# Optimization experiments

Measured on AMD Instinct MI355X. Metric: run time of the kernel, lower is better.

## Reference

```python
import jax, jax.numpy as jnp
import numpy as np

ALPHA = 0.3  # LeakyReLU negative slope
NEG_INF = -1e9


def setup_inputs() -> dict:
    key = jax.random.key(0)
    k1, k2, k3, k4 = jax.random.split(key, 4)
    B, N, C_IN, C_OUT, H = 4, 2048, 128, 128, 4
    node_feats = jax.random.normal(k1, (B, N, C_IN), dtype=jnp.float32)
    # xavier_uniform with gain 1.414 for projection weight [c_out, c_in]
    limit_w = 1.414 * np.sqrt(6.0 / (C_IN + C_OUT))
    W = jax.random.uniform(k2, (C_OUT, C_IN), minval=-limit_w, maxval=limit_w, dtype=jnp.float32)
    b = jnp.zeros((C_OUT,), dtype=jnp.float32)
    c_head = C_OUT // H
    limit_a = 1.414 * np.sqrt(6.0 / (H + 2 * c_head))
    a = jax.random.uniform(k3, (H, 2 * c_head), minval=-limit_a, maxval=limit_a, dtype=jnp.float32)
    return {"node_feats": node_feats, "W": W, "b": b, "a": a}


def reference(node_feats, W, b, a):
    B, N, _ = node_feats.shape
    H, two_c = a.shape
    c = two_c // 2
    # dynamic adjacency: cosine similarity, sigmoid > 0.5  <=>  sim > 0
    nf = node_feats / jnp.maximum(jnp.linalg.norm(node_feats, axis=-1, keepdims=True), 1e-12)
    sim = jnp.einsum('bid,bjd->bij', nf, nf)            # [B,N,N]
    mask = sim > 0.0                                     # adjacency (sigmoid(sim) > 0.5)
    # projection -> per-head features [B,N,H,c]
    h = (node_feats @ W.T + b).reshape(B, N, H, c)
    # edge score a . [h_i, h_j] decomposes into left/right parts
    a_l, a_r = a[:, :c], a[:, c:]                        # [H,c] each
    s_l = jnp.einsum('bnhc,hc->bnh', h, a_l)             # [B,N,H]
    s_r = jnp.einsum('bnhc,hc->bnh', h, a_r)             # [B,N,H]
    logits = jax.nn.leaky_relu(s_l[:, :, None, :] + s_r[:, None, :, :], ALPHA)  # [B,N,N,H]
    attn = jnp.where(mask[..., None], logits, NEG_INF)
    probs = jax.nn.softmax(attn, axis=2)                 # softmax over source nodes j
    # dropout is identity in eval mode
    out = jnp.einsum('bijh,bjhc->bihc', probs, h)
    return out.reshape(B, N, -1)                         # concat heads
```

## Files before the change

### kernel.cpp

```cpp
#include <hip/hip_runtime.h>
#include <cstdint>
#include <cstddef>

typedef float v16f __attribute__((ext_vector_type(16)));
typedef short v8s  __attribute__((ext_vector_type(8)));

#define MFMA32(A,B,C) __builtin_amdgcn_mfma_f32_32x32x16_bf16((A),(B),(C),0,0,0)
#define THRU 1e-3f

__device__ __forceinline__ unsigned f2bf(float f) {
  unsigned u = __builtin_bit_cast(unsigned, f);
  u += 0x7FFFu + ((u >> 16) & 1u);
  return u >> 16;
}
__device__ __forceinline__ float bf2f(unsigned us) {
  return __builtin_bit_cast(float, us << 16);
}
__device__ __forceinline__ void gload16(const void* g, void* l) {
  __builtin_amdgcn_global_load_lds(
      (const __attribute__((address_space(1))) void*)g,
      (__attribute__((address_space(3))) void*)l, 16, 0, 0);
}

__global__ __launch_bounds__(256) void gat_prep(
    const float* __restrict__ nf, const float* __restrict__ Wm,
    const float* __restrict__ bias, const float* __restrict__ aw,
    unsigned short* __restrict__ nfh, unsigned short* __restrict__ nfm,
    unsigned short* __restrict__ ht,
    float* __restrict__ EFl, float* __restrict__ EFrp)
{
  __shared__ float xl[32][132];
  const int tid = threadIdx.x;
  const int row = tid & 31, g = tid >> 5;
  const int r0 = blockIdx.x * 32;
  const int b = r0 >> 11, n0 = r0 & 2047;
  const int d0 = g * 16;

  float x[16];
  {
    const float* xp = nf + (size_t)(r0 + row) * 128 + d0;
#pragma unroll
    for (int q = 0; q < 4; ++q) {
      float4 v = *(const float4*)(xp + 4 * q);
      x[4*q+0] = v.x; x[4*q+1] = v.y; x[4*q+2] = v.z; x[4*q+3] = v.w;
    }
  }
  {
    unsigned hu[16], mu[16];
#pragma unroll
    for (int q = 0; q < 16; ++q) {
      xl[row][d0 + q] = x[q];
      unsigned hb = f2bf(x[q]); float hf = bf2f(hb);
      unsigned mb = f2bf(x[q] - hf);
      hu[q] = hb; mu[q] = mb;
    }
    const size_t to = ((size_t)(b * 64 + (n0 >> 5)) * 8 + g) * 512 + row * 8;
    uint4 p0, p1;
    p0.x = hu[0] | (hu[1] << 16);  p0.y = hu[2] | (hu[3] << 16);
    p0.z = hu[4] | (hu[5] << 16);  p0.w = hu[6] | (hu[7] << 16);
    p1.x = hu[8] | (hu[9] << 16);  p1.y = hu[10] | (hu[11] << 16);
    p1.z = hu[12] | (hu[13] << 16); p1.w = hu[14] | (hu[15] << 16);
    *(uint4*)(nfh + to) = p0; *(uint4*)(nfh + to + 256) = p1;
    p0.x = mu[0] | (mu[1] << 16);  p0.y = mu[2] | (mu[3] << 16);
    p0.z = mu[4] | (mu[5] << 16);  p0.w = mu[6] | (mu[7] << 16);
    p1.x = mu[8] | (mu[9] << 16);  p1.y = mu[10] | (mu[11] << 16);
    p1.z = mu[12] | (mu[13] << 16); p1.w = mu[14] | (mu[15] << 16);
    *(uint4*)(nfm + to) = p0; *(uint4*)(nfm + to + 256) = p1;
  }
  __syncthreads();

  float acc[16];
  const int ob = g * 16;
#pragma unroll
  for (int o = 0; o < 16; ++o) acc[o] = bias[ob + o];
  for (int dd = 0; dd < 128; dd += 4) {
    float4 xq = *(const float4*)&xl[row][dd];
#pragma unroll
    for (int o = 0; o < 16; ++o) {
      float4 wq = *(const float4*)(Wm + (size_t)(ob + o) * 128 + dd);
      acc[o] = fmaf(xq.x, wq.x, acc[o]);
      acc[o] = fmaf(xq.y, wq.y, acc[o]);
      acc[o] = fmaf(xq.z, wq.z, acc[o]);
      acc[o] = fmaf(xq.w, wq.w, acc[o]);
    }
  }
#pragma unroll
  for (int o = 0; o < 16; ++o)
    ht[((size_t)b * 128 + ob + o) * 2048 + n0 + row] = (unsigned short)f2bf(acc[o]);

  const int hh = g >> 1, cb = (g & 1) * 16;
  float sl = 0.f, sr = 0.f;
#pragma unroll
  for (int o = 0; o < 16; ++o) {
    sl = fmaf(acc[o], aw[hh * 64 + cb + o], sl);
    sr = fmaf(acc[o], aw[hh * 64 + 32 + cb + o], sr);
  }
  sl += __shfl_xor(sl, 32, 64);
  sr += __shfl_xor(sr, 32, 64);
  if (!(g & 1)) {
    const float L2E = 1.4426950408889634f;
    float El = exp2f(sl * L2E), Fl = exp2f(sl * (0.3f * L2E));
    float Er = exp2f(sr * L2E), Fr = exp2f(sr * (0.3f * L2E));
    size_t nn = (size_t)(r0 + row);
    EFl[nn * 8 + hh]     = El;
    EFl[nn * 8 + 4 + hh] = Fl;
    EFrp[nn * 8 + (hh >> 1) * 4 + (hh & 1) * 2]     = Er;
    EFrp[nn * 8 + (hh >> 1) * 4 + (hh & 1) * 2 + 1] = Fr;
  }
}

__global__ __launch_bounds__(256) void gat_mask(
    const unsigned short* __restrict__ nfh, const unsigned short* __restrict__ nfm,
    const float* __restrict__ nf, unsigned* __restrict__ mask)
{
  const int tid = threadIdx.x, lane = tid & 63;
  const int li = lane & 31, hi = lane >> 5;
  const int blk = blockIdx.x;
  const int jb = blk & 31, t = blk >> 5;
  const int ib = t & 15, b = t >> 4;
  const int i0 = ib * 128 + (tid >> 6) * 32;
  const int j0 = jb * 64;

  const size_t lbyte = (size_t)lane * 8;
  const size_t tiB  = ((size_t)(b * 64 + (i0 >> 5)) * 8) * 512 + lbyte;
  const size_t tjA0 = ((size_t)(b * 64 + (j0 >> 5)) * 8) * 512 + lbyte;
  const size_t tjA1 = tjA0 + 4096;

  v8s BH[8], BM[8];
#pragma unroll
  for (int kc = 0; kc < 8; ++kc) {
    BH[kc] = *(const v8s*)(nfh + tiB + kc * 512);
    BM[kc] = *(const v8s*)(nfm + tiB + kc * 512);
  }

  v16f S0, S1;
#pragma unroll
  for (int r = 0; r < 16; ++r) { S0[r] = 0.f; S1[r] = 0.f; }
#pragma unroll
  for (int kc = 0; kc < 8; ++kc) {
    v8s A0h = *(const v8s*)(nfh + tjA0 + kc * 512);
    v8s A1h = *(const v8s*)(nfh + tjA1 + kc * 512);
    v8s A0m = *(const v8s*)(nfm + tjA0 + kc * 512);
    v8s A1m = *(const v8s*)(nfm + tjA1 + kc * 512);
    S0 = MFMA32(A0h, BH[kc], S0);
    S1 = MFMA32(A1h, BH[kc], S1);
    S0 = MFMA32(A0h, BM[kc], S0);
    S1 = MFMA32(A1h, BM[kc], S1);
    S0 = MFMA32(A0m, BH[kc], S0);
    S1 = MFMA32(A1m, BH[kc], S1);
  }

  unsigned u0 = 0, u1 = 0;
  float mn = 1e30f;
  const int sh = hi * 4;
#pragma unroll
  for (int r = 0; r < 16; ++r) {
    const int jlc = (r & 3) + 8 * (r >> 2);
    const unsigned bit = (1u << jlc) << sh;
    if (S0[r] > 0.f) u0 |= bit;
    if (S1[r] > 0.f) u1 |= bit;
    mn = fminf(mn, fabsf(S0[r]));
    mn = fminf(mn, fabsf(S1[r]));
  }

  if (mn < THRU) {
    const float* xi = nf + ((size_t)b * 2048 + i0 + li) * 128;
#pragma unroll
    for (int sub = 0; sub < 2; ++sub) {
#pragma unroll
      for (int r = 0; r < 16; ++r) {
        const float s = sub ? S1[r] : S0[r];
        if (fabsf(s) < THRU) {
          const int jlc = (r & 3) + 8 * (r >> 2);
          const int j = j0 + sub * 32 + jlc + 4 * hi;
          const float* xj = nf + ((size_t)b * 2048 + j) * 128;
          double a = 0.0;
          for (int k = 0; k < 128; k += 2) {
            a = fma((double)xi[k],     (double)xj[k],     a);
            a = fma((double)xi[k + 1], (double)xj[k + 1], a);
          }
          const unsigned bit = (1u << jlc) << sh;
          if (sub == 0) u0 = (a > 0.0) ? (u0 | bit) : (u0 & ~bit);
          else          u1 = (a > 0.0) ? (u1 | bit) : (u1 & ~bit);
        }
      }
    }
  }

  unsigned f0 = u0 | (unsigned)__shfl_xor((int)u0, 32, 64);
  unsigned f1 = u1 | (unsigned)__shfl_xor((int)u1, 32, 64);
  if (hi == 0) {
    mask[(size_t)(b * 64 + jb * 2)     * 2048 + i0 + li] = f0;
    mask[(size_t)(b * 64 + jb * 2 + 1) * 2048 + i0 + li] = f1;
  }
}

#define PVBLK(pw, h, smv)                                                      \
  {                                                                            \
    auto q0 = __builtin_amdgcn_permlane32_swap((int)pw[0], (int)pw[2], false, false); \
    auto q1 = __builtin_amdgcn_permlane32_swap((int)pw[1], (int)pw[3], false, false); \
    auto q2 = __builtin_amdgcn_permlane32_swap((int)pw[4], (int)pw[6], false, false); \
    auto q3 = __builtin_amdgcn_permlane32_swap((int)pw[5], (int)pw[7], false, false); \
    uint4 c0, c1;                                                              \
    c0.x = (unsigned)q0[0]; c0.y = (unsigned)q1[0];                            \
    c0.z = (unsigned)q0[1]; c0.w = (unsigned)q1[1];                            \
    c1.x = (unsigned)q2[0]; c1.y = (unsigned)q3[0];                            \
    c1.z = (unsigned)q2[1]; c1.w = (unsigned)q3[1];                            \
    v8s P0 = __builtin_bit_cast(v8s, c0);                                      \
    v8s P1 = __builtin_bit_cast(v8s, c1);                                      \
    const int cc = (h) * 32 + li;                                              \
    const char* vr = (smv) + cc * 256;                                         \
    const int cx = cc & 15;                                                    \
    v8s V0 = *(const v8s*)(vr + ((((it2 << 2) + hi) ^ cx) << 4));              \
    v8s V1 = *(const v8s*)(vr + ((((it2 << 2) + 2 + hi) ^ cx) << 4));          \
    acc[h] = MFMA32(P0, V0, acc[h]);                                           \
    acc[h] = MFMA32(P1, V1, acc[h]);                                           \
  }

template<int CH>
__global__ __launch_bounds__(256, 2) void gat_attn(
    const unsigned short* __restrict__ ht, const float* __restrict__ EFl,
    const float* __restrict__ EFrp, const unsigned* __restrict__ mask,
    float* __restrict__ nump, float* __restrict__ denp)
{
  constexpr int JPC = 2048 / CH;
  constexpr int H = JPC >> 7;
  constexpr int MW = JPC >> 5;
  __shared__ __align__(16) char sm[2][18432];

  const int tid = threadIdx.x, lane = tid & 63, wv = tid >> 6;
  const int li = lane & 31, hi = lane >> 5;

  const int blk = blockIdx.x;
  const int x = blk & 7, y = blk >> 3;
  const int ig = y & 15;
  const int combo = x * CH + (y >> 4);
  const int hp2 = combo & 1;
  const int r2 = combo >> 1;
  const int ch = r2 % CH, b = r2 / CH;

  const size_t nb = (size_t)b * 2048;
  const int i0 = ig * 128 + wv * 32;
  const int j0 = ch * JPC;

  float EL[2], FL[2];
  {
    const float* p = EFl + (nb + i0 + li) * 8 + 2 * hp2;
    float2 e = *(const float2*)p;
    float2 f = *(const float2*)(p + 4);
    EL[0] = e.x; EL[1] = e.y; FL[0] = f.x; FL[1] = f.y;
  }

  unsigned mw[MW];
#pragma unroll
  for (int q = 0; q < MW; ++q)
    mw[q] = mask[(size_t)(b * 64 + (j0 >> 5) + q) * 2048 + i0 + li] >> (hi * 4);

  v16f acc[2];
#pragma unroll
  for (int h = 0; h < 2; ++h)
#pragma unroll
    for (int r = 0; r < 16; ++r) acc[h][r] = 0.f;
  float den[2] = {0.f, 0.f};

  auto STAGE = [&](int h0, int p) {
    const int jbase = j0 + (h0 << 7);
    const size_t cbase = (size_t)b * 128 + (hp2 << 6);
#pragma unroll
    for (int s = 0; s < 4; ++s) {
      const int L = s * 4096 + tid * 16;
      const int c = L >> 8, gs = (L >> 4) & 15;
      const int g = gs ^ (c & 15);
      gload16((const char*)ht + (((cbase + c) * 2048 + jbase) << 1) + (g << 4),
              sm[p] + L);
    }
    if (tid < 128)
      gload16((const char*)EFrp + (size_t)(nb + jbase + tid) * 32 + (hp2 << 4),
              sm[p] + 16384 + tid * 16);
  };

  STAGE(0, 0);
  __syncthreads();

#pragma unroll
  for (int h0 = 0; h0 < H; ++h0) {
    const int p = h0 & 1;
    if (h0) __syncthreads();
    if (h0 + 1 < H) STAGE(h0 + 1, p ^ 1);

#pragma unroll
    for (int it2 = 0; it2 < 4; ++it2) {
      const char* Eb = sm[p] + 16384 + (it2 << 9);
      const unsigned mh = mw[(h0 << 2) + it2];
      unsigned pA[8], pB[8];
#pragma unroll
      for (int rp = 0; rp < 8; ++rp) {
        const int r0 = 2 * rp;
        const int jl0c = (r0 & 3) + 8 * (r0 >> 2);
        const int nA = (jl0c + 4 * hi) * 16;
        float4 e0 = *(const float4*)(Eb + nA);
        float4 e1 = *(const float4*)(Eb + nA + 16);
        const bool m0 = (mh >> jl0c) & 1;
        const bool m1 = (mh >> (jl0c + 1)) & 1;
        float wA0 = fmaxf(e0.x * EL[0], e0.y * FL[0]); wA0 = m0 ? wA0 : 0.f;
        float wB0 = fmaxf(e0.z * EL[1], e0.w * FL[1]); wB0 = m0 ? wB0 : 0.f;
        float wA1 = fmaxf(e1.x * EL[0], e1.y * FL[0]); wA1 = m1 ? wA1 : 0.f;
        float wB1 = fmaxf(e1.z * EL[1], e1.w * FL[1]); wB1 = m1 ? wB1 : 0.f;
        den[0] += wA0 + wA1;
        den[1] += wB0 + wB1;
        asm("v_cvt_pk_bf16_f32 %0, %1, %2" : "=v"(pA[rp]) : "v"(wA0), "v"(wA1));
        asm("v_cvt_pk_bf16_f32 %0, %1, %2" : "=v"(pB[rp]) : "v"(wB0), "v"(wB1));
      }
      PVBLK(pA, 0, sm[p])
      PVBLK(pB, 1, sm[p])
    }
  }

#pragma unroll
  for (int h = 0; h < 2; ++h) den[h] += __shfl_xor(den[h], 32, 64);

  const size_t obase = ((size_t)b * CH + ch) * 2048 + i0;
#pragma unroll
  for (int h = 0; h < 2; ++h) {
#pragma unroll
    for (int r = 0; r < 16; ++r) {
      const int il = (r & 3) + 8 * (r >> 2) + 4 * hi;
      nump[(obase + il) * 128 + (hp2 * 2 + h) * 32 + li] = acc[h][r];
    }
  }
  if (lane < 32) {
    float2 dv; dv.x = den[0]; dv.y = den[1];
    *(float2*)(denp + (obase + li) * 4 + 2 * hp2) = dv;
  }
}

__global__ __launch_bounds__(256) void gat_reduce(
    const float* __restrict__ nump, const float* __restrict__ denp,
    float* __restrict__ out, const int CH)
{
  const int t = blockIdx.x * 256 + threadIdx.x;
  const int b = t >> 16;
  const int rem = t & 65535;
  const int n = rem >> 5;
  const int col = (rem & 31) * 4;
  const int h = col >> 5;
  float4 s = make_float4(0.f, 0.f, 0.f, 0.f);
  float d = 0.f;
  for (int ch = 0; ch < CH; ++ch) {
    const size_t rb = ((size_t)b * CH + ch) * 2048 + n;
    float4 v = *(const float4*)(nump + rb * 128 + col);
    s.x += v.x; s.y += v.y; s.z += v.z; s.w += v.w;
    d += denp[rb * 4 + h];
  }
  float4 o;
  o.x = s.x / d; o.y = s.y / d; o.z = s.z / d; o.w = s.w / d;
  *(float4*)(out + (size_t)t * 4) = o;
}

extern "C" void kernel_launch(void* const* d_in, const int* in_sizes, int n_in,
                              void* d_out, int out_size, void* d_ws, size_t ws_size,
                              hipStream_t stream) {
  const float* nf   = (const float*)d_in[0];
  const float* Wm   = (const float*)d_in[1];
  const float* bias = (const float*)d_in[2];
  const float* aw   = (const float*)d_in[3];
  float* out = (float*)d_out;
  char* ws = (char*)d_ws;

  unsigned short* nfh  = (unsigned short*)(ws);
  unsigned short* nfm  = (unsigned short*)(ws + 2097152);
  unsigned short* ht   = (unsigned short*)(ws + 4194304);
  float*    EFl  = (float*)(ws + 6291456);
  float*    EFrp = (float*)(ws + 6553600);
  unsigned* mask = (unsigned*)(ws + 6815744);
  const size_t o_den = 8912896;

  int CH = 8;
  if (ws_size < o_den + 8ull * 4325376ull) CH = 4;

  float* denp = (float*)(ws + o_den);
  float* nump = (float*)(ws + o_den + (size_t)CH * 131072);

  gat_prep<<<256, 256, 0, stream>>>(nf, Wm, bias, aw, nfh, nfm, ht, EFl, EFrp);
  gat_mask<<<2048, 256, 0, stream>>>(nfh, nfm, nf, mask);
  if (CH == 8)
    gat_attn<8><<<1024, 256, 0, stream>>>(ht, EFl, EFrp, mask, nump, denp);
  else
    gat_attn<4><<<512, 256, 0, stream>>>(ht, EFl, EFrp, mask, nump, denp);
  gat_reduce<<<1024, 256, 0, stream>>>(nump, denp, out, CH);
}
```

Measured before the change: 76.24 us.

## Pre-tile projected features in MFMA operand layout, load V directly to registers

The projection kernel now writes h in a layout pre-swizzled to match the 32x32x16 MFMA B-operand fragment, so the attention kernel loads V straight from global memory into registers. This removes the double-buffered LDS staging of V and its per-stage barriers; only the EFrp right-side factors are staged, once. Separately, the mask kernel now processes two j-blocks per workgroup with half the grid, reusing the i-side operands held in registers. The trade is more global load latency exposed in the attention loop, with no LDS buffering to hide it.

Result: slower. 84.37 us (+10.7%).

```diff
diff --git a/kernel.cpp b/kernel.cpp
--- a/kernel.cpp
+++ b/kernel.cpp
@@ -26,7 +26,7 @@
     const float* __restrict__ nf, const float* __restrict__ Wm,
     const float* __restrict__ bias, const float* __restrict__ aw,
     unsigned short* __restrict__ nfh, unsigned short* __restrict__ nfm,
-    unsigned short* __restrict__ ht,
+    unsigned short* __restrict__ vt,
     float* __restrict__ EFl, float* __restrict__ EFrp)
 {
   __shared__ float xl[32][132];
@@ -84,9 +84,16 @@
       acc[o] = fmaf(xq.w, wq.w, acc[o]);
     }
   }
-#pragma unroll
-  for (int o = 0; o < 16; ++o)
-    ht[((size_t)b * 128 + ob + o) * 2048 + n0 + row] = (unsigned short)f2bf(acc[o]);
+  {
+    const int f = (row >> 4) & 1, kh = (row >> 3) & 1, e = row & 7;
+#pragma unroll
+    for (int o = 0; o < 16; ++o) {
+      const int c = ob + o, hh2 = c >> 5, cc = c & 31;
+      const size_t va = (((size_t)(b * 4 + hh2) * 64 + (n0 >> 5)) * 2 + f) * 512
+                        + (kh * 32 + cc) * 8 + e;
+      vt[va] = (unsigned short)f2bf(acc[o]);
+    }
+  }
 
   const int hh = g >> 1, cb = (g & 1) * 16;
   float sl = 0.f, sr = 0.f;
@@ -116,15 +123,12 @@
   const int tid = threadIdx.x, lane = tid & 63;
   const int li = lane & 31, hi = lane >> 5;
   const int blk = blockIdx.x;
-  const int jb = blk & 31, t = blk >> 5;
+  const int jb2 = blk & 15, t = blk >> 4;
   const int ib = t & 15, b = t >> 4;
   const int i0 = ib * 128 + (tid >> 6) * 32;
-  const int j0 = jb * 64;
 
   const size_t lbyte = (size_t)lane * 8;
-  const size_t tiB  = ((size_t)(b * 64 + (i0 >> 5)) * 8) * 512 + lbyte;
-  const size_t tjA0 = ((size_t)(b * 64 + (j0 >> 5)) * 8) * 512 + lbyte;
-  const size_t tjA1 = tjA0 + 4096;
+  const size_t tiB = ((size_t)(b * 64 + (i0 >> 5)) * 8) * 512 + lbyte;
 
   v8s BH[8], BM[8];
 #pragma unroll
@@ -132,70 +136,77 @@
     BH[kc] = *(const v8s*)(nfh + tiB + kc * 512);
     BM[kc] = *(const v8s*)(nfm + tiB + kc * 512);
   }
-
-  v16f S0, S1;
-#pragma unroll
-  for (int r = 0; r < 16; ++r) { S0[r] = 0.f; S1[r] = 0.f; }
-#pragma unroll
-  for (int kc = 0; kc < 8; ++kc) {
-    v8s A0h = *(const v8s*)(nfh + tjA0 + kc * 512);
-    v8s A1h = *(const v8s*)(nfh + tjA1 + kc * 512);
-    v8s A0m = *(const v8s*)(nfm + tjA0 + kc * 512);
-    v8s A1m = *(const v8s*)(nfm + tjA1 + kc * 512);
-    S0 = MFMA32(A0h, BH[kc], S0);
-    S1 = MFMA32(A1h, BH[kc], S1);
-    S0 = MFMA32(A0h, BM[kc], S0);
-    S1 = MFMA32(A1h, BM[kc], S1);
-    S0 = MFMA32(A0m, BH[kc], S0);
-    S1 = MFMA32(A1m, BH[kc], S1);
-  }
-
-  unsigned u0 = 0, u1 = 0;
-  float mn = 1e30f;
+  const float* xi = nf + ((size_t)b * 2048 + i0 + li) * 128;
   const int sh = hi * 4;
-#pragma unroll
-  for (int r = 0; r < 16; ++r) {
-    const int jlc = (r & 3) + 8 * (r >> 2);
-    const unsigned bit = (1u << jlc) << sh;
-    if (S0[r] > 0.f) u0 |= bit;
-    if (S1[r] > 0.f) u1 |= bit;
-    mn = fminf(mn, fabsf(S0[r]));
-    mn = fminf(mn, fabsf(S1[r]));
-  }
-
-  if (mn < THRU) {
-    const float* xi = nf + ((size_t)b * 2048 + i0 + li) * 128;
-#pragma unroll
-    for (int sub = 0; sub < 2; ++sub) {
-#pragma unroll
-      for (int r = 0; r < 16; ++r) {
-        const float s = sub ? S1[r] : S0[r];
-        if (fabsf(s) < THRU) {
-          const int jlc = (r & 3) + 8 * (r >> 2);
-          const int j = j0 + sub * 32 + jlc + 4 * hi;
-          const float* xj = nf + ((size_t)b * 2048 + j) * 128;
-          double a = 0.0;
-          for (int k = 0; k < 128; k += 2) {
-            a = fma((double)xi[k],     (double)xj[k],     a);
-            a = fma((double)xi[k + 1], (double)xj[k + 1], a);
+
+  for (int jj = 0; jj < 2; ++jj) {
+    const int jb = jb2 * 2 + jj;
+    const int j0 = jb * 64;
+    const size_t tjA0 = ((size_t)(b * 64 + (j0 >> 5)) * 8) * 512 + lbyte;
+    const size_t tjA1 = tjA0 + 4096;
+
+    v16f S0, S1;
+#pragma unroll
+    for (int r = 0; r < 16; ++r) { S0[r] = 0.f; S1[r] = 0.f; }
+#pragma unroll
+    for (int kc = 0; kc < 8; ++kc) {
+      v8s A0h = *(const v8s*)(nfh + tjA0 + kc * 512);
+      v8s A1h = *(const v8s*)(nfh + tjA1 + kc * 512);
+      v8s A0m = *(const v8s*)(nfm + tjA0 + kc * 512);
+      v8s A1m = *(const v8s*)(nfm + tjA1 + kc * 512);
+      S0 = MFMA32(A0h, BH[kc], S0);
+      S1 = MFMA32(A1h, BH[kc], S1);
+      S0 = MFMA32(A0h, BM[kc], S0);
+      S1 = MFMA32(A1h, BM[kc], S1);
+      S0 = MFMA32(A0m, BH[kc], S0);
+      S1 = MFMA32(A1m, BH[kc], S1);
+    }
+
+    unsigned u0 = 0, u1 = 0;
+    float mn = 1e30f;
+#pragma unroll
+    for (int r = 0; r < 16; ++r) {
+      const int jlc = (r & 3) + 8 * (r >> 2);
+      const unsigned bit = (1u << jlc) << sh;
+      if (S0[r] > 0.f) u0 |= bit;
+      if (S1[r] > 0.f) u1 |= bit;
+      mn = fminf(mn, fabsf(S0[r]));
+      mn = fminf(mn, fabsf(S1[r]));
+    }
+
+    if (mn < THRU) {
+#pragma unroll
+      for (int sub = 0; sub < 2; ++sub) {
+#pragma unroll
+        for (int r = 0; r < 16; ++r) {
+          const float s = sub ? S1[r] : S0[r];
+          if (fabsf(s) < THRU) {
+            const int jlc = (r & 3) + 8 * (r >> 2);
+            const int j = j0 + sub * 32 + jlc + 4 * hi;
+            const float* xj = nf + ((size_t)b * 2048 + j) * 128;
+            double a = 0.0;
+            for (int k = 0; k < 128; k += 2) {
+              a = fma((double)xi[k],     (double)xj[k],     a);
+              a = fma((double)xi[k + 1], (double)xj[k + 1], a);
+            }
+            const unsigned bit = (1u << jlc) << sh;
+            if (sub == 0) u0 = (a > 0.0) ? (u0 | bit) : (u0 & ~bit);
+            else          u1 = (a > 0.0) ? (u1 | bit) : (u1 & ~bit);
           }
-          const unsigned bit = (1u << jlc) << sh;
-          if (sub == 0) u0 = (a > 0.0) ? (u0 | bit) : (u0 & ~bit);
-          else          u1 = (a > 0.0) ? (u1 | bit) : (u1 & ~bit);
         }
       }
     }
-  }
-
-  unsigned f0 = u0 | (unsigned)__shfl_xor((int)u0, 32, 64);
-  unsigned f1 = u1 | (unsigned)__shfl_xor((int)u1, 32, 64);
-  if (hi == 0) {
-    mask[(size_t)(b * 64 + jb * 2)     * 2048 + i0 + li] = f0;
-    mask[(size_t)(b * 64 + jb * 2 + 1) * 2048 + i0 + li] = f1;
-  }
-}
-
-#define PVBLK(pw, h, smv)                                                      \
+
+    unsigned f0 = u0 | (unsigned)__shfl_xor((int)u0, 32, 64);
+    unsigned f1 = u1 | (unsigned)__shfl_xor((int)u1, 32, 64);
+    if (hi == 0) {
+      mask[(size_t)(b * 64 + jb * 2)     * 2048 + i0 + li] = f0;
+      mask[(size_t)(b * 64 + jb * 2 + 1) * 2048 + i0 + li] = f1;
+    }
+  }
+}
+
+#define PVREG(pw, h, Va, Vb)                                                   \
   {                                                                            \
     auto q0 = __builtin_amdgcn_permlane32_swap((int)pw[0], (int)pw[2], false, false); \
     auto q1 = __builtin_amdgcn_permlane32_swap((int)pw[1], (int)pw[3], false, false); \
@@ -208,25 +219,19 @@
     c1.z = (unsigned)q2[1]; c1.w = (unsigned)q3[1];                            \
     v8s P0 = __builtin_bit_cast(v8s, c0);                                      \
     v8s P1 = __builtin_bit_cast(v8s, c1);                                      \
-    const int cc = (h) * 32 + li;                                              \
-    const char* vr = (smv) + cc * 256;                                         \
-    const int cx = cc & 15;                                                    \
-    v8s V0 = *(const v8s*)(vr + ((((it2 << 2) + hi) ^ cx) << 4));              \
-    v8s V1 = *(const v8s*)(vr + ((((it2 << 2) + 2 + hi) ^ cx) << 4));          \
-    acc[h] = MFMA32(P0, V0, acc[h]);                                           \
-    acc[h] = MFMA32(P1, V1, acc[h]);                                           \
+    acc[h] = MFMA32(P0, (Va), acc[h]);                                         \
+    acc[h] = MFMA32(P1, (Vb), acc[h]);                                         \
   }
 
 template<int CH>
 __global__ __launch_bounds__(256, 2) void gat_attn(
-    const unsigned short* __restrict__ ht, const float* __restrict__ EFl,
+    const unsigned short* __restrict__ vt, const float* __restrict__ EFl,
     const float* __restrict__ EFrp, const unsigned* __restrict__ mask,
     float* __restrict__ nump, float* __restrict__ denp)
 {
   constexpr int JPC = 2048 / CH;
-  constexpr int H = JPC >> 7;
-  constexpr int MW = JPC >> 5;
-  __shared__ __align__(16) char sm[2][18432];
+  constexpr int NT = JPC >> 5;
+  __shared__ __align__(16) char sm[JPC * 16];
 
   const int tid = threadIdx.x, lane = tid & 63, wv = tid >> 6;
   const int li = lane & 31, hi = lane >> 5;
@@ -251,10 +256,14 @@
     EL[0] = e.x; EL[1] = e.y; FL[0] = f.x; FL[1] = f.y;
   }
 
-  unsigned mw[MW];
-#pragma unroll
-  for (int q = 0; q < MW; ++q)
+  unsigned mw[NT];
+#pragma unroll
+  for (int q = 0; q < NT; ++q)
     mw[q] = mask[(size_t)(b * 64 + (j0 >> 5) + q) * 2048 + i0 + li] >> (hi * 4);
+
+  for (int q = tid; q < JPC; q += 256)
+    gload16((const char*)EFrp + (size_t)(nb + j0 + q) * 32 + (hp2 << 4),
+            sm + q * 16);
 
   v16f acc[2];
 #pragma unroll
@@ -263,57 +272,41 @@
     for (int r = 0; r < 16; ++r) acc[h][r] = 0.f;
   float den[2] = {0.f, 0.f};
 
-  auto STAGE = [&](int h0, int p) {
-    const int jbase = j0 + (h0 << 7);
-    const size_t cbase = (size_t)b * 128 + (hp2 << 6);
-#pragma unroll
-    for (int s = 0; s < 4; ++s) {
-      const int L = s * 4096 + tid * 16;
-      const int c = L >> 8, gs = (L >> 4) & 15;
-      const int g = gs ^ (c & 15);
-      gload16((const char*)ht + (((cbase + c) * 2048 + jbase) << 1) + (g << 4),
-              sm[p] + L);
-    }
-    if (tid < 128)
-      gload16((const char*)EFrp + (size_t)(nb + jbase + tid) * 32 + (hp2 << 4),
-              sm[p] + 16384 + tid * 16);
-  };
-
-  STAGE(0, 0);
+  const unsigned short* vb0 =
+      vt + ((size_t)(b * 4 + 2 * hp2) * 64 + (j0 >> 5)) * 1024 + (size_t)lane * 8;
+  const unsigned short* vb1 = vb0 + 65536;
+
   __syncthreads();
 
-#pragma unroll
-  for (int h0 = 0; h0 < H; ++h0) {
-    const int p = h0 & 1;
-    if (h0) __syncthreads();
-    if (h0 + 1 < H) STAGE(h0 + 1, p ^ 1);
-
-#pragma unroll
-    for (int it2 = 0; it2 < 4; ++it2) {
-      const char* Eb = sm[p] + 16384 + (it2 << 9);
-      const unsigned mh = mw[(h0 << 2) + it2];
-      unsigned pA[8], pB[8];
-#pragma unroll
-      for (int rp = 0; rp < 8; ++rp) {
-        const int r0 = 2 * rp;
-        const int jl0c = (r0 & 3) + 8 * (r0 >> 2);
-        const int nA = (jl0c + 4 * hi) * 16;
-        float4 e0 = *(const float4*)(Eb + nA);
-        float4 e1 = *(const float4*)(Eb + nA + 16);
-        const bool m0 = (mh >> jl0c) & 1;
-        const bool m1 = (mh >> (jl0c + 1)) & 1;
-        float wA0 = fmaxf(e0.x * EL[0], e0.y * FL[0]); wA0 = m0 ? wA0 : 0.f;
-        float wB0 = fmaxf(e0.z * EL[1], e0.w * FL[1]); wB0 = m0 ? wB0 : 0.f;
-        float wA1 = fmaxf(e1.x * EL[0], e1.y * FL[0]); wA1 = m1 ? wA1 : 0.f;
-        float wB1 = fmaxf(e1.z * EL[1], e1.w * FL[1]); wB1 = m1 ? wB1 : 0.f;
-        den[0] += wA0 + wA1;
-        den[1] += wB0 + wB1;
-        asm("v_cvt_pk_bf16_f32 %0, %1, %2" : "=v"(pA[rp]) : "v"(wA0), "v"(wA1));
-        asm("v_cvt_pk_bf16_f32 %0, %1, %2" : "=v"(pB[rp]) : "v"(wB0), "v"(wB1));
-      }
-      PVBLK(pA, 0, sm[p])
-      PVBLK(pB, 1, sm[p])
-    }
+#pragma unroll 2
+  for (int it2 = 0; it2 < NT; ++it2) {
+    const unsigned mh = mw[it2];
+    v8s V00 = *(const v8s*)(vb0 + it2 * 1024);
+    v8s V01 = *(const v8s*)(vb0 + it2 * 1024 + 512);
+    v8s V10 = *(const v8s*)(vb1 + it2 * 1024);
+    v8s V11 = *(const v8s*)(vb1 + it2 * 1024 + 512);
+    const char* Eb = sm + (it2 << 9);
+    unsigned pA[8], pB[8];
+#pragma unroll
+    for (int rp = 0; rp < 8; ++rp) {
+      const int r0 = 2 * rp;
+      const int jl0c = (r0 & 3) + 8 * (r0 >> 2);
+      const int nA = (jl0c + 4 * hi) * 16;
+      float4 e0 = *(const float4*)(Eb + nA);
+      float4 e1 = *(const float4*)(Eb + nA + 16);
+      const bool m0 = (mh >> jl0c) & 1;
+      const bool m1 = (mh >> (jl0c + 1)) & 1;
+      float wA0 = fmaxf(e0.x * EL[0], e0.y * FL[0]); wA0 = m0 ? wA0 : 0.f;
+      float wB0 = fmaxf(e0.z * EL[1], e0.w * FL[1]); wB0 = m0 ? wB0 : 0.f;
+      float wA1 = fmaxf(e1.x * EL[0], e1.y * FL[0]); wA1 = m1 ? wA1 : 0.f;
+      float wB1 = fmaxf(e1.z * EL[1], e1.w * FL[1]); wB1 = m1 ? wB1 : 0.f;
+      den[0] += wA0 + wA1;
+      den[1] += wB0 + wB1;
+      asm("v_cvt_pk_bf16_f32 %0, %1, %2" : "=v"(pA[rp]) : "v"(wA0), "v"(wA1));
+      asm("v_cvt_pk_bf16_f32 %0, %1, %2" : "=v"(pB[rp]) : "v"(wB0), "v"(wB1));
+    }
+    PVREG(pA, 0, V00, V01)
+    PVREG(pB, 1, V10, V11)
   }
 
 #pragma unroll
@@ -369,7 +362,7 @@
 
   unsigned short* nfh  = (unsigned short*)(ws);
   unsigned short* nfm  = (unsigned short*)(ws + 2097152);
-  unsigned short* ht   = (unsigned short*)(ws + 4194304);
+  unsigned short* vt   = (unsigned short*)(ws + 4194304);
   float*    EFl  = (float*)(ws + 6291456);
   float*    EFrp = (float*)(ws + 6553600);
   unsigned* mask = (unsigned*)(ws + 6815744);
@@ -381,11 +374,11 @@
   float* denp = (float*)(ws + o_den);
   float* nump = (float*)(ws + o_den + (size_t)CH * 131072);
 
-  gat_prep<<<256, 256, 0, stream>>>(nf, Wm, bias, aw, nfh, nfm, ht, EFl, EFrp);
-  gat_mask<<<2048, 256, 0, stream>>>(nfh, nfm, nf, mask);
+  gat_prep<<<256, 256, 0, stream>>>(nf, Wm, bias, aw, nfh, nfm, vt, EFl, EFrp);
+  gat_mask<<<1024, 256, 0, stream>>>(nfh, nfm, nf, mask);
   if (CH == 8)
-    gat_attn<8><<<1024, 256, 0, stream>>>(ht, EFl, EFrp, mask, nump, denp);
+    gat_attn<8><<<1024, 256, 0, stream>>>(vt, EFl, EFrp, mask, nump, denp);
   else
-    gat_attn<4><<<512, 256, 0, stream>>>(ht, EFl, EFrp, mask, nump, denp);
+    gat_attn<4><<<512, 256, 0, stream>>>(vt, EFl, EFrp, mask, nump, denp);
   gat_reduce<<<1024, 256, 0, stream>>>(nump, denp, out, CH);
 }
```
